# Kernel tuning notes

Hardware: AMD Instinct MI355X
Metric: run time of the kernel (lower is better)

Reference implementation:

```python
import jax, jax.numpy as jnp
import numpy as np


def setup_inputs() -> dict:
    key = jax.random.key(0)
    k1, k2, k3 = jax.random.split(key, 3)
    B, Tc, Tq, D = 8, 4096, 1024, 256
    context = jax.random.normal(k1, (B, Tc, D), dtype=jnp.float32)
    question = jax.random.normal(k2, (B, Tq, D), dtype=jnp.float32)
    w = jax.random.normal(k3, (3 * D, 1), dtype=jnp.float32) * 0.05
    return {"context": context, "question": question, "w": w}


def reference(context, question, w):
    # context: (B, Tc, D); question: (B, Tq, D); w: (3D, 1)
    D = context.shape[-1]
    w1, w2, w3 = w[:D, 0], w[D:2 * D, 0], w[2 * D:, 0]
    # Fused similarity: S[b,i,j] = w1.c_i + w2.q_j + w3.(c_i*q_j)
    # (mathematically identical to the tiled concat + linear score, but
    # avoids materializing the (B,Tc,Tq,3D) tensor)
    s_c = jnp.einsum('bid,d->bi', context, w1)              # (B, Tc)
    s_q = jnp.einsum('bjd,d->bj', question, w2)             # (B, Tq)
    s_cq = jnp.einsum('bid,bjd->bij', context * w3, question)  # (B, Tc, Tq)
    S = s_cq + s_c[:, :, None] + s_q[:, None, :]
    A = jax.nn.softmax(S, axis=-1)                           # (B, Tc, Tq)
    # C2Q attention: U[b,i] = sum_j A[b,i,j] * q_j
    U = jnp.einsum('bij,bjd->bid', A, question)              # (B, Tc, D)
    # Q2C attention: b_i = max_j A[b,i,j]; h = sum_i b_i * c_i, tiled over Tc
    b = jnp.max(A, axis=-1)                                  # (B, Tc)
    h = jnp.einsum('bi,bid->bd', b, context)                 # (B, D)
    H = jnp.broadcast_to(h[:, None, :], context.shape)       # (B, Tc, D)
    # megamerge
    G = jnp.concatenate([context, U, context * U, context * H], axis=-1)
    return G  # (B, Tc, 4D)
```

## Files before the change

### kernel.cpp

```cpp
#include <hip/hip_runtime.h>
#include <hip/hip_bf16.h>
#include <stdint.h>
#include <stddef.h>


#define NB 8
#define TC 4096
#define TQ 1024
#define DD 256
#define JT 32
#define NJT (TQ / JT)

typedef __attribute__((ext_vector_type(4)))  float  f32x4v;
typedef __attribute__((ext_vector_type(8)))  __bf16 bf16x8v;
typedef __attribute__((ext_vector_type(4)))  __bf16 bf16x4v;

#define QA_OFF   0
#define QX_OFF   (QA_OFF + NB*NJT*16*1024)
#define SQ_OFF   (QX_OFF + NB*NJT*16*1024)
#define HV_OFF   (SQ_OFF + NB*TQ*4)

__device__ __forceinline__ void async_cp16(const void* g, void* l) {
  __builtin_amdgcn_global_load_lds(
      (const __attribute__((address_space(1))) void*)g,
      (__attribute__((address_space(3))) void*)l, 16, 0, 0);
}

__global__ __launch_bounds__(256) void k_qprep(const float* __restrict__ question,
                                               const float* __restrict__ w,
                                               char* __restrict__ ws) {
  uint4* qa = (uint4*)(ws + QA_OFF);
  uint4* qx = (uint4*)(ws + QX_OFF);
  float* sq = (float*)(ws + SQ_OFF);
  __shared__ __align__(16) __bf16 T[32][264];

  int bx = blockIdx.x;
  int b = bx >> 5, it = bx & 31;
  int t = threadIdx.x;
  int j = t >> 3;
  int seg = t & 7;

  const float* qrow = question + ((size_t)(b * TQ + it * JT + j)) * DD + seg * 32;
  const float* w2 = w + DD;

  float part = 0.f;
#pragma unroll
  for (int k = 0; k < 8; ++k) {
    float4 v  = *(const float4*)(qrow + 4 * k);
    float4 wv = *(const float4*)(w2 + seg * 32 + 4 * k);
    part += v.x * wv.x + v.y * wv.y + v.z * wv.z + v.w * wv.w;
    bf16x4v pk = {(__bf16)v.x, (__bf16)v.y, (__bf16)v.z, (__bf16)v.w};
    *(bf16x4v*)&T[j][seg * 32 + 4 * k] = pk;
  }
  part += __shfl_xor(part, 1);
  part += __shfl_xor(part, 2);
  part += __shfl_xor(part, 4);
  if (seg == 0) sq[b * TQ + it * JT + j] = part;
  __syncthreads();

#pragma unroll
  for (int p = 0; p < 4; ++p) {
    int ch = t + 256 * p;
    int L = ch & 63, cc = ch >> 6;
    int jm = cc >> 3, c = cc & 7;
    int nh = L & 15, qh = L >> 4;
    uint4 v = *(const uint4*)&T[16 * jm + nh][32 * c + 8 * qh];
    qa[(size_t)(b * NJT + it) * 1024 + ch] = v;
  }
#pragma unroll
  for (int p = 0; p < 4; ++p) {
    int ch = t + 256 * p;
    int L = ch & 63, mt = ch >> 6;
    int nh = L & 15, qh = L >> 4;
    __bf16 e[8];
#pragma unroll
    for (int o = 0; o < 8; ++o) e[o] = T[8 * qh + o][16 * mt + nh];
    qx[(size_t)(b * NJT + it) * 1024 + ch] = *(const uint4*)e;
  }
}

__global__ __launch_bounds__(256, 2) void k_main(const float* __restrict__ context,
                                                 const float* __restrict__ w,
                                                 const char* __restrict__ ws,
                                                 float* __restrict__ hv,
                                                 float* __restrict__ out) {
  const uint4*  qa = (const uint4*)(ws + QA_OFF);
  const __bf16* qx = (const __bf16*)(ws + QX_OFF);
  const float*  sq = (const float*)(ws + SQ_OFF);

  __shared__ __align__(16) __bf16 qa_lds[2][8192];
  __shared__ __align__(16) __bf16 pa_lds[2][4][16][40];
  __shared__ __align__(16) float  sq_all[TQ];
  __shared__ __align__(16) float  red_lm[2][4][16][2];
  __shared__ __align__(16) float  rinv_lds[64];
  __shared__ __align__(16) float  bvv_lds[64];

  int bx = blockIdx.x;
  int b = bx & 7;
  int ig = bx >> 3;
  int t = threadIdx.x;
  int wv = t >> 6;
  int lane = t & 63;
  int wi = wv >> 1;
  int wj = wv & 1;
  int it0 = 2 * wi, it1 = 2 * wi + 1;
  int nh = lane & 15;
  int qh = lane >> 4;

  const uint4* qa_b = qa + (size_t)b * NJT * 1024;
  const __bf16* qx_b = qx + (size_t)b * NJT * 8192;
  const float* sqb = sq + b * TQ;

  bf16x8v cw3f0[8], cw3f1[8];
  {
    const float* crow0 = context + ((size_t)(b * TC + ig * 64 + 32 * wi + nh)) * DD;
    const float* crow1 = crow0 + 16 * DD;
    const float* w3 = w + 2 * DD;
#pragma unroll
    for (int c = 0; c < 8; ++c) {
      int d0 = 32 * c + 8 * qh;
      float4 g0 = *(const float4*)(w3 + d0);
      float4 g1 = *(const float4*)(w3 + d0 + 4);
      float4 f0 = *(const float4*)(crow0 + d0);
      float4 f1 = *(const float4*)(crow0 + d0 + 4);
      bf16x8v fr;
      fr[0] = (__bf16)(f0.x * g0.x); fr[1] = (__bf16)(f0.y * g0.y);
      fr[2] = (__bf16)(f0.z * g0.z); fr[3] = (__bf16)(f0.w * g0.w);
      fr[4] = (__bf16)(f1.x * g1.x); fr[5] = (__bf16)(f1.y * g1.y);
      fr[6] = (__bf16)(f1.z * g1.z); fr[7] = (__bf16)(f1.w * g1.w);
      cw3f0[c] = fr;
      float4 h0 = *(const float4*)(crow1 + d0);
      float4 h1 = *(const float4*)(crow1 + d0 + 4);
      bf16x8v hr;
      hr[0] = (__bf16)(h0.x * g0.x); hr[1] = (__bf16)(h0.y * g0.y);
      hr[2] = (__bf16)(h0.z * g0.z); hr[3] = (__bf16)(h0.w * g0.w);
      hr[4] = (__bf16)(h1.x * g1.x); hr[5] = (__bf16)(h1.y * g1.y);
      hr[6] = (__bf16)(h1.z * g1.z); hr[7] = (__bf16)(h1.w * g1.w);
      cw3f1[c] = hr;
    }
  }

  {
    ((float4*)sq_all)[t] = ((const float4*)sqb)[t];
    const uint4* src = qa_b;
#pragma unroll
    for (int p = 0; p < 4; ++p) {
      int cb = wv * 64 + p * 256;
      async_cp16(src + cb + lane, &qa_lds[0][(size_t)cb * 8]);
    }
  }

  f32x4v U[16];
#pragma unroll
  for (int k = 0; k < 16; ++k) U[k] = (f32x4v){0.f, 0.f, 0.f, 0.f};
  float m0_run = -1e30f, l0_run = 0.f;
  float m1_run = -1e30f, l1_run = 0.f;

  __syncthreads();

  {
    {
      const uint4* src = qa_b + 1024;
#pragma unroll
      for (int p = 0; p < 4; ++p) {
        int cb = wv * 64 + p * 256;
        async_cp16(src + cb + lane, &qa_lds[1][(size_t)cb * 8]);
      }
    }
    f32x4v S0 = {0.f, 0.f, 0.f, 0.f}, S1 = {0.f, 0.f, 0.f, 0.f};
#pragma unroll
    for (int c = 0; c < 8; ++c) {
      bf16x8v ac = *(const bf16x8v*)&qa_lds[0][((wj * 8 + c) * 64 + lane) * 8];
      S0 = __builtin_amdgcn_mfma_f32_16x16x32_bf16(ac, cw3f0[c], S0, 0, 0, 0);
      S1 = __builtin_amdgcn_mfma_f32_16x16x32_bf16(ac, cw3f1[c], S1, 0, 0, 0);
    }
    float4 sqv = *(const float4*)&sq_all[16 * wj + 4 * qh];
    float a0 = S0[0] + sqv.x, a1 = S0[1] + sqv.y, a2 = S0[2] + sqv.z, a3 = S0[3] + sqv.w;
    float b0 = S1[0] + sqv.x, b1 = S1[1] + sqv.y, b2 = S1[2] + sqv.z, b3 = S1[3] + sqv.w;
    float e0 = __expf(a0), e1 = __expf(a1), e2 = __expf(a2), e3 = __expf(a3);
    float f0 = __expf(b0), f1 = __expf(b1), f2 = __expf(b2), f3 = __expf(b3);
    m0_run = fmaxf(m0_run, fmaxf(fmaxf(a0, a1), fmaxf(a2, a3)));
    m1_run = fmaxf(m1_run, fmaxf(fmaxf(b0, b1), fmaxf(b2, b3)));
    l0_run += (e0 + e1) + (e2 + e3);
    l1_run += (f0 + f1) + (f2 + f3);
    bf16x4v pk0 = {(__bf16)e0, (__bf16)e1, (__bf16)e2, (__bf16)e3};
    bf16x4v pk1 = {(__bf16)f0, (__bf16)f1, (__bf16)f2, (__bf16)f3};
    *(bf16x4v*)&pa_lds[0][it0][nh][16 * wj + 4 * qh] = pk0;
    *(bf16x4v*)&pa_lds[0][it1][nh][16 * wj + 4 * qh] = pk1;
    __syncthreads();
  }

  for (int itq = 1; itq < NJT; ++itq) {
    int cur = itq & 1;

    bf16x8v bqr[4];
    {
      const __bf16* qxt = qx_b + (size_t)(itq - 1) * 8192 + lane * 8;
#pragma unroll
      for (int nt = 0; nt < 4; ++nt)
        bqr[nt] = *(const bf16x8v*)(qxt + (size_t)(wv * 4 + nt) * 512);
    }

    if (itq + 1 < NJT) {
      const uint4* src = qa_b + (size_t)(itq + 1) * 1024;
#pragma unroll
      for (int p = 0; p < 4; ++p) {
        int cb = wv * 64 + p * 256;
        async_cp16(src + cb + lane, &qa_lds[cur ^ 1][(size_t)cb * 8]);
      }
    }

    f32x4v S0 = {0.f, 0.f, 0.f, 0.f}, S1 = {0.f, 0.f, 0.f, 0.f};
#pragma unroll
    for (int c = 0; c < 8; ++c) {
      bf16x8v ac = *(const bf16x8v*)&qa_lds[cur][((wj * 8 + c) * 64 + lane) * 8];
      S0 = __builtin_amdgcn_mfma_f32_16x16x32_bf16(ac, cw3f0[c], S0, 0, 0, 0);
      S1 = __builtin_amdgcn_mfma_f32_16x16x32_bf16(ac, cw3f1[c], S1, 0, 0, 0);
    }

#pragma unroll
    for (int mi = 0; mi < 4; ++mi) {
      bf16x8v af = *(const bf16x8v*)&pa_lds[cur ^ 1][mi][nh][8 * qh];
#pragma unroll
      for (int nt = 0; nt < 4; ++nt)
        U[mi * 4 + nt] = __builtin_amdgcn_mfma_f32_16x16x32_bf16(af, bqr[nt], U[mi * 4 + nt], 0, 0, 0);
    }

    float4 sqv = *(const float4*)&sq_all[itq * JT + 16 * wj + 4 * qh];
    float a0 = S0[0] + sqv.x, a1 = S0[1] + sqv.y, a2 = S0[2] + sqv.z, a3 = S0[3] + sqv.w;
    float b0 = S1[0] + sqv.x, b1 = S1[1] + sqv.y, b2 = S1[2] + sqv.z, b3 = S1[3] + sqv.w;
    float e0 = __expf(a0), e1 = __expf(a1), e2 = __expf(a2), e3 = __expf(a3);
    float f0 = __expf(b0), f1 = __expf(b1), f2 = __expf(b2), f3 = __expf(b3);
    m0_run = fmaxf(m0_run, fmaxf(fmaxf(a0, a1), fmaxf(a2, a3)));
    m1_run = fmaxf(m1_run, fmaxf(fmaxf(b0, b1), fmaxf(b2, b3)));
    l0_run += (e0 + e1) + (e2 + e3);
    l1_run += (f0 + f1) + (f2 + f3);

    bf16x4v pk0 = {(__bf16)e0, (__bf16)e1, (__bf16)e2, (__bf16)e3};
    bf16x4v pk1 = {(__bf16)f0, (__bf16)f1, (__bf16)f2, (__bf16)f3};
    *(bf16x4v*)&pa_lds[cur][it0][nh][16 * wj + 4 * qh] = pk0;
    *(bf16x4v*)&pa_lds[cur][it1][nh][16 * wj + 4 * qh] = pk1;

    __syncthreads();
  }

  {
    bf16x8v bqr[4];
    const __bf16* qxt = qx_b + (size_t)(NJT - 1) * 8192 + lane * 8;
#pragma unroll
    for (int nt = 0; nt < 4; ++nt)
      bqr[nt] = *(const bf16x8v*)(qxt + (size_t)(wv * 4 + nt) * 512);
#pragma unroll
    for (int mi = 0; mi < 4; ++mi) {
      bf16x8v af = *(const bf16x8v*)&pa_lds[(NJT - 1) & 1][mi][nh][8 * qh];
#pragma unroll
      for (int nt = 0; nt < 4; ++nt)
        U[mi * 4 + nt] = __builtin_amdgcn_mfma_f32_16x16x32_bf16(af, bqr[nt], U[mi * 4 + nt], 0, 0, 0);
    }
  }

  float lo0 = l0_run + __shfl_xor(l0_run, 16); lo0 += __shfl_xor(lo0, 32);
  float lo1 = l1_run + __shfl_xor(l1_run, 16); lo1 += __shfl_xor(lo1, 32);
  float mo0 = fmaxf(m0_run, __shfl_xor(m0_run, 16)); mo0 = fmaxf(mo0, __shfl_xor(mo0, 32));
  float mo1 = fmaxf(m1_run, __shfl_xor(m1_run, 16)); mo1 = fmaxf(mo1, __shfl_xor(mo1, 32));
  if (lane < 16) {
    red_lm[wj][it0][nh][0] = lo0; red_lm[wj][it0][nh][1] = mo0;
    red_lm[wj][it1][nh][0] = lo1; red_lm[wj][it1][nh][1] = mo1;
  }
  __syncthreads();
  if (t < 64) {
    int it = t >> 4, n = t & 15;
    float l = red_lm[0][it][n][0] + red_lm[1][it][n][0];
    float m = fmaxf(red_lm[0][it][n][1], red_lm[1][it][n][1]);
    float ri = 1.0f / l;
    rinv_lds[t] = ri;
    bvv_lds[t] = __expf(m) * ri;
  }
  __syncthreads();

  float hacc[4] = {0.f, 0.f, 0.f, 0.f};
#pragma unroll
  for (int mi = 0; mi < 4; ++mi) {
#pragma unroll
    for (int r = 0; r < 4; ++r) {
      int rl = mi * 16 + 4 * qh + r;
      int row = ig * 64 + rl;
      float rv = rinv_lds[rl];
      float bb = bvv_lds[rl];
      const float* crow = context + ((size_t)(b * TC + row)) * DD;
      float* orow = out + ((size_t)(b * TC + row)) * (4 * DD);
#pragma unroll
      for (int nt = 0; nt < 4; ++nt) {
        int d = wv * 64 + nt * 16 + nh;
        float c = crow[d];
        float u = U[mi * 4 + nt][r] * rv;
        orow[d] = c;
        orow[DD + d] = u;
        orow[2 * DD + d] = c * u;
        hacc[nt] += bb * c;
      }
    }
  }
#pragma unroll
  for (int nt = 0; nt < 4; ++nt) {
    float h = hacc[nt] + __shfl_xor(hacc[nt], 16);
    h += __shfl_xor(h, 32);
    if (qh == 0) atomicAdd(&hv[b * DD + wv * 64 + nt * 16 + nh], h);
  }
}

__global__ __launch_bounds__(256) void k_final(const float* __restrict__ context,
                                               const char* __restrict__ ws,
                                               float* __restrict__ out) {
  const float* hv = (const float*)(ws + HV_OFF);
  int gid = blockIdx.x * 256 + threadIdx.x;
  int row = gid >> 6;
  int d = (gid & 63) * 4;
  int b = row >> 12;
  float4 c4 = ((const float4*)context)[gid];
  float4 h4 = *(const float4*)(hv + b * DD + d);
  float4 r;
  r.x = c4.x * h4.x; r.y = c4.y * h4.y; r.z = c4.z * h4.z; r.w = c4.w * h4.w;
  *(float4*)(out + (size_t)row * TQ + 3 * DD + d) = r;
}

extern "C" void kernel_launch(void* const* d_in, const int* in_sizes, int n_in,
                              void* d_out, int out_size, void* d_ws, size_t ws_size,
                              hipStream_t stream) {
  (void)in_sizes; (void)n_in; (void)out_size; (void)ws_size;
  const float* context  = (const float*)d_in[0];
  const float* question = (const float*)d_in[1];
  const float* w        = (const float*)d_in[2];
  float* out = (float*)d_out;
  char* ws = (char*)d_ws;

  k_qprep<<<NB * NJT, 256, 0, stream>>>(question, w, ws);
  hipMemsetAsync(ws + HV_OFF, 0, NB * DD * sizeof(float), stream);
  k_main<<<NB * (TC / 64), 256, 0, stream>>>(context, w, ws,
                                             (float*)(ws + HV_OFF), out);
  k_final<<<(NB * TC * DD / 4) / 256, 256, 0, stream>>>(context, ws, out);
}
```

Baseline: 212.0 us.

## Load question A-fragments directly into registers instead of staging through LDS

Removes the double-buffered LDS staging of the pre-packed question fragments. Each wave now loads its own MFMA A-operands from global memory straight into registers, prefetching the next tile while the current S-tile MFMAs run. This frees 32KB of LDS and drops the async copies, possibly allowing more occupancy. The block barrier is replaced with an inline s_waitcnt lgkmcnt(0) plus s_barrier, so the barrier no longer waits on outstanding global loads (vmcnt). The cost is more VGPR pressure and duplicate global loads across waves that share the same wj.

```diff
diff --git a/kernel.cpp b/kernel.cpp
--- a/kernel.cpp
+++ b/kernel.cpp
@@ -19,12 +19,6 @@
 #define QX_OFF   (QA_OFF + NB*NJT*16*1024)
 #define SQ_OFF   (QX_OFF + NB*NJT*16*1024)
 #define HV_OFF   (SQ_OFF + NB*TQ*4)
-
-__device__ __forceinline__ void async_cp16(const void* g, void* l) {
-  __builtin_amdgcn_global_load_lds(
-      (const __attribute__((address_space(1))) void*)g,
-      (__attribute__((address_space(3))) void*)l, 16, 0, 0);
-}
 
 __global__ __launch_bounds__(256) void k_qprep(const float* __restrict__ question,
                                                const float* __restrict__ w,
@@ -88,7 +82,6 @@
   const __bf16* qx = (const __bf16*)(ws + QX_OFF);
   const float*  sq = (const float*)(ws + SQ_OFF);
 
-  __shared__ __align__(16) __bf16 qa_lds[2][8192];
   __shared__ __align__(16) __bf16 pa_lds[2][4][16][40];
   __shared__ __align__(16) float  sq_all[TQ];
   __shared__ __align__(16) float  red_lm[2][4][16][2];
@@ -110,6 +103,8 @@
   const uint4* qa_b = qa + (size_t)b * NJT * 1024;
   const __bf16* qx_b = qx + (size_t)b * NJT * 8192;
   const float* sqb = sq + b * TQ;
+
+  const uint4* qa_w = qa_b + (size_t)wj * 512 + lane;
 
   bf16x8v cw3f0[8], cw3f1[8];
   {
@@ -140,15 +135,11 @@
     }
   }
 
-  {
-    ((float4*)sq_all)[t] = ((const float4*)sqb)[t];
-    const uint4* src = qa_b;
-#pragma unroll
-    for (int p = 0; p < 4; ++p) {
-      int cb = wv * 64 + p * 256;
-      async_cp16(src + cb + lane, &qa_lds[0][(size_t)cb * 8]);
-    }
-  }
+  ((float4*)sq_all)[t] = ((const float4*)sqb)[t];
+
+  bf16x8v afr[8];
+#pragma unroll
+  for (int c = 0; c < 8; ++c) afr[c] = *(const bf16x8v*)(qa_w + c * 64);
 
   f32x4v U[16];
 #pragma unroll
@@ -159,21 +150,15 @@
   __syncthreads();
 
   {
-    {
-      const uint4* src = qa_b + 1024;
-#pragma unroll
-      for (int p = 0; p < 4; ++p) {
-        int cb = wv * 64 + p * 256;
-        async_cp16(src + cb + lane, &qa_lds[1][(size_t)cb * 8]);
-      }
-    }
     f32x4v S0 = {0.f, 0.f, 0.f, 0.f}, S1 = {0.f, 0.f, 0.f, 0.f};
 #pragma unroll
     for (int c = 0; c < 8; ++c) {
-      bf16x8v ac = *(const bf16x8v*)&qa_lds[0][((wj * 8 + c) * 64 + lane) * 8];
-      S0 = __builtin_amdgcn_mfma_f32_16x16x32_bf16(ac, cw3f0[c], S0, 0, 0, 0);
-      S1 = __builtin_amdgcn_mfma_f32_16x16x32_bf16(ac, cw3f1[c], S1, 0, 0, 0);
-    }
+      S0 = __builtin_amdgcn_mfma_f32_16x16x32_bf16(afr[c], cw3f0[c], S0, 0, 0, 0);
+      S1 = __builtin_amdgcn_mfma_f32_16x16x32_bf16(afr[c], cw3f1[c], S1, 0, 0, 0);
+    }
+#pragma unroll
+    for (int c = 0; c < 8; ++c) afr[c] = *(const bf16x8v*)(qa_w + 1024 + c * 64);
+
     float4 sqv = *(const float4*)&sq_all[16 * wj + 4 * qh];
     float a0 = S0[0] + sqv.x, a1 = S0[1] + sqv.y, a2 = S0[2] + sqv.z, a3 = S0[3] + sqv.w;
     float b0 = S1[0] + sqv.x, b1 = S1[1] + sqv.y, b2 = S1[2] + sqv.z, b3 = S1[3] + sqv.w;
@@ -187,7 +172,7 @@
     bf16x4v pk1 = {(__bf16)f0, (__bf16)f1, (__bf16)f2, (__bf16)f3};
     *(bf16x4v*)&pa_lds[0][it0][nh][16 * wj + 4 * qh] = pk0;
     *(bf16x4v*)&pa_lds[0][it1][nh][16 * wj + 4 * qh] = pk1;
-    __syncthreads();
+    asm volatile("s_waitcnt lgkmcnt(0)\n\ts_barrier" ::: "memory");
   }
 
   for (int itq = 1; itq < NJT; ++itq) {
@@ -201,21 +186,17 @@
         bqr[nt] = *(const bf16x8v*)(qxt + (size_t)(wv * 4 + nt) * 512);
     }
 
+    f32x4v S0 = {0.f, 0.f, 0.f, 0.f}, S1 = {0.f, 0.f, 0.f, 0.f};
+#pragma unroll
+    for (int c = 0; c < 8; ++c) {
+      S0 = __builtin_amdgcn_mfma_f32_16x16x32_bf16(afr[c], cw3f0[c], S0, 0, 0, 0);
+      S1 = __builtin_amdgcn_mfma_f32_16x16x32_bf16(afr[c], cw3f1[c], S1, 0, 0, 0);
+    }
+
     if (itq + 1 < NJT) {
-      const uint4* src = qa_b + (size_t)(itq + 1) * 1024;
-#pragma unroll
-      for (int p = 0; p < 4; ++p) {
-        int cb = wv * 64 + p * 256;
-        async_cp16(src + cb + lane, &qa_lds[cur ^ 1][(size_t)cb * 8]);
-      }
-    }
-
-    f32x4v S0 = {0.f, 0.f, 0.f, 0.f}, S1 = {0.f, 0.f, 0.f, 0.f};
-#pragma unroll
-    for (int c = 0; c < 8; ++c) {
-      bf16x8v ac = *(const bf16x8v*)&qa_lds[cur][((wj * 8 + c) * 64 + lane) * 8];
-      S0 = __builtin_amdgcn_mfma_f32_16x16x32_bf16(ac, cw3f0[c], S0, 0, 0, 0);
-      S1 = __builtin_amdgcn_mfma_f32_16x16x32_bf16(ac, cw3f1[c], S1, 0, 0, 0);
+#pragma unroll
+      for (int c = 0; c < 8; ++c)
+        afr[c] = *(const bf16x8v*)(qa_w + (size_t)(itq + 1) * 1024 + c * 64);
     }
 
 #pragma unroll
@@ -241,7 +222,7 @@
     *(bf16x4v*)&pa_lds[cur][it0][nh][16 * wj + 4 * qh] = pk0;
     *(bf16x4v*)&pa_lds[cur][it1][nh][16 * wj + 4 * qh] = pk1;
 
-    __syncthreads();
+    asm volatile("s_waitcnt lgkmcnt(0)\n\ts_barrier" ::: "memory");
   }
 
   {
```

Measured after the change: 204.1 us. 3.7% less time.
